# Kernel optimization log

Measured on AMD Instinct MI355X. Metric: run time of the kernel, lower is better.

Reference implementation:

```python
import jax, jax.numpy as jnp
import numpy as np
from jax import lax

EPS = 1e-5

def _layernorm(x, g, b):
    m = jnp.mean(x, axis=-1, keepdims=True)
    v = jnp.mean((x - m) ** 2, axis=-1, keepdims=True)
    return (x - m) * lax.rsqrt(v + EPS) * g + b

def _dwconv(x, H, W, w, b):
    # x: [B, N, C], w: [C, 1, 3, 3] (OIHW, depthwise), b: [C]
    B, N, C = x.shape
    xi = x.transpose(0, 2, 1).reshape(B, C, H, W)
    y = lax.conv_general_dilated(
        xi, w, window_strides=(1, 1), padding='SAME',
        feature_group_count=C,
        dimension_numbers=('NCHW', 'OIHW', 'NCHW'))
    y = y + b[None, :, None, None]
    return y.reshape(B, C, H * W).transpose(0, 2, 1)

def _channel_attn(x, groups, qkv_w, qkv_b, proj_w, proj_b):
    B, N, C = x.shape
    hd = C // groups
    qkv = x @ qkv_w.T + qkv_b                       # [B, N, 3C]
    qkv = qkv.reshape(B, N, 3, groups, hd)
    q, k, v = qkv[:, :, 0], qkv[:, :, 1], qkv[:, :, 2]   # [B, N, g, hd]
    q = q * (float(N) ** -0.5)
    attn = jnp.einsum('bngc,bngd->bgcd', q, k)      # [B, g, hd, hd]
    attn = jax.nn.softmax(attn, axis=-1)
    out = jnp.einsum('bgcd,bngd->bngc', attn, v)    # [B, N, g, hd]
    out = out.reshape(B, N, C)
    return out @ proj_w.T + proj_b

def _block(x, H, W, dw1_w, dw1_b, ln1_g, ln1_b, qkv_w, qkv_b, proj_w, proj_b,
           dw2_w, dw2_b, ln2_g, ln2_b, fc1_w, fc1_b, fc2_w, fc2_b, groups=8):
    # conv1 (no norm) + residual
    x = x + _dwconv(x, H, W, dw1_w, dw1_b)
    # prenorm channel attention + residual
    x = x + _channel_attn(_layernorm(x, ln1_g, ln1_b), groups, qkv_w, qkv_b, proj_w, proj_b)
    # conv2 (no norm) + residual
    x = x + _dwconv(x, H, W, dw2_w, dw2_b)
    # prenorm MLP + residual
    h = _layernorm(x, ln2_g, ln2_b)
    h = jax.nn.gelu(h @ fc1_w.T + fc1_b, approximate=False)
    x = x + (h @ fc2_w.T + fc2_b)
    return x

def setup_inputs() -> dict:
    key = jax.random.key(0)
    B, H, W, C, groups, ratio = 32, 32, 32, 768, 8, 4
    N, Ch = H * W, C * ratio
    ks = jax.random.split(key, 16)
    s = lambda fan: 1.0 / np.sqrt(fan)
    return {
        'x': jax.random.normal(ks[0], (B, N, C), jnp.float32),
        'H': H, 'W': W,
        'dw1_w': jax.random.normal(ks[1], (C, 1, 3, 3), jnp.float32) * s(9),
        'dw1_b': jnp.zeros((C,), jnp.float32),
        'ln1_g': jnp.ones((C,), jnp.float32),
        'ln1_b': jnp.zeros((C,), jnp.float32),
        'qkv_w': jax.random.normal(ks[2], (3 * C, C), jnp.float32) * s(C),
        'qkv_b': jnp.zeros((3 * C,), jnp.float32),
        'proj_w': jax.random.normal(ks[3], (C, C), jnp.float32) * s(C),
        'proj_b': jnp.zeros((C,), jnp.float32),
        'dw2_w': jax.random.normal(ks[4], (C, 1, 3, 3), jnp.float32) * s(9),
        'dw2_b': jnp.zeros((C,), jnp.float32),
        'ln2_g': jnp.ones((C,), jnp.float32),
        'ln2_b': jnp.zeros((C,), jnp.float32),
        'fc1_w': jax.random.normal(ks[5], (Ch, C), jnp.float32) * s(C),
        'fc1_b': jnp.zeros((Ch,), jnp.float32),
        'fc2_w': jax.random.normal(ks[6], (C, Ch), jnp.float32) * s(Ch),
        'fc2_b': jnp.zeros((C,), jnp.float32),
    }

def reference(x, H, W, dw1_w, dw1_b, ln1_g, ln1_b, qkv_w, qkv_b, proj_w, proj_b,
              dw2_w, dw2_b, ln2_g, ln2_b, fc1_w, fc1_b, fc2_w, fc2_b):
    return _block(x, H, W, dw1_w, dw1_b, ln1_g, ln1_b, qkv_w, qkv_b, proj_w, proj_b,
                  dw2_w, dw2_b, ln2_g, ln2_b, fc1_w, fc1_b, fc2_w, fc2_b)
```

## Files before the change

### kernel.cpp

```cpp
#include <hip/hip_runtime.h>

typedef unsigned short ushort_t;
typedef __bf16 v8bf __attribute__((ext_vector_type(8)));
typedef float v4f __attribute__((ext_vector_type(4)));

#define B_ 32
#define N_ 1024
#define C_ 768
#define G_ 8
#define HD_ 96
#define CH_ 3072
#define M_ 32768

static __device__ __forceinline__ float b2f(ushort_t u) {
    union { float f; unsigned int i; } z; z.i = ((unsigned int)u) << 16; return z.f;
}
static __device__ __forceinline__ ushort_t f2b(float f) {
    unsigned int u = __float_as_uint(f);
    u += 0x7fff + ((u >> 16) & 1);
    return (ushort_t)(u >> 16);
}
static __device__ __forceinline__ unsigned int pk2(float a, float b) {
    return (unsigned int)f2b(a) | ((unsigned int)f2b(b) << 16);
}

#define GLOAD_LDS16(g, l) __builtin_amdgcn_global_load_lds( \
    (const __attribute__((address_space(1))) unsigned int*)(g), \
    (__attribute__((address_space(3))) unsigned int*)(l), 16, 0, 0)

__global__ __launch_bounds__(256) void cvt_bf16(
    const float* __restrict__ in, ushort_t* __restrict__ out)
{
    int i = (blockIdx.x * 256 + threadIdx.x) * 4;
    float4 v = *(const float4*)(in + i);
    uint2 p; p.x = pk2(v.x, v.y); p.y = pk2(v.z, v.w);
    *(uint2*)(out + i) = p;
}

__global__ __launch_bounds__(256) void transpose_w(
    const float* __restrict__ w, float* __restrict__ wt)
{
    int i = blockIdx.x * 256 + threadIdx.x;
    int c = i / 9, k = i % 9;
    wt[k * C_ + c] = w[i];
}

__global__ __launch_bounds__(256) void dwconv_add(
    const float* __restrict__ xin, const float* __restrict__ wt,
    const float* __restrict__ bias, float* __restrict__ out)
{
    int t = threadIdx.x;
    int bid = blockIdx.x;
    int cblk = bid % 6;
    int bh = bid / 6;
    int b = bh >> 5, h = bh & 31;
    int tw = t >> 5;
    int c0 = cblk * 128 + (t & 31) * 4;
    int w0 = tw * 4;

    float4 tap[3][6];
#pragma unroll
    for (int dh = 0; dh < 3; dh++) {
        int hh = h + dh - 1;
        bool hok = (hh >= 0) && (hh < 32);
#pragma unroll
        for (int dw = 0; dw < 6; dw++) {
            int ww = w0 + dw - 1;
            bool ok = hok && (ww >= 0) && (ww < 32);
            if (ok)
                tap[dh][dw] = *(const float4*)(
                    xin + (size_t)((b << 10) | (hh << 5) | ww) * C_ + c0);
            else
                tap[dh][dw] = make_float4(0.f, 0.f, 0.f, 0.f);
        }
    }
    float4 wv[9];
#pragma unroll
    for (int k = 0; k < 9; k++)
        wv[k] = *(const float4*)(wt + k * C_ + c0);
    float4 bv = *(const float4*)(bias + c0);

#pragma unroll
    for (int i = 0; i < 4; i++) {
        float4 acc = bv;
#pragma unroll
        for (int dh = 0; dh < 3; dh++)
#pragma unroll
            for (int dw = 0; dw < 3; dw++) {
                float4 xv = tap[dh][i + dw];
                float4 wk = wv[dh * 3 + dw];
                acc.x += wk.x * xv.x; acc.y += wk.y * xv.y;
                acc.z += wk.z * xv.z; acc.w += wk.w * xv.w;
            }
        float4 xr = tap[1][i + 1];
        acc.x += xr.x; acc.y += xr.y; acc.z += xr.z; acc.w += xr.w;
        *(float4*)(out + (size_t)((b << 10) | (h << 5) | (w0 + i)) * C_ + c0) = acc;
    }
}

__global__ __launch_bounds__(256) void layernorm_bf(
    const float* __restrict__ xin, const float* __restrict__ g,
    const float* __restrict__ bb, ushort_t* __restrict__ out)
{
    int row = blockIdx.x;
    int t = threadIdx.x;
    const float* xr = xin + (size_t)row * C_;
    float x0 = xr[t], x1 = xr[t + 256], x2 = xr[t + 512];
    float s1 = x0 + x1 + x2;
    float s2 = x0 * x0 + x1 * x1 + x2 * x2;
#pragma unroll
    for (int o = 32; o > 0; o >>= 1) {
        s1 += __shfl_xor(s1, o);
        s2 += __shfl_xor(s2, o);
    }
    __shared__ float red[8];
    if ((t & 63) == 0) { red[(t >> 6) * 2] = s1; red[(t >> 6) * 2 + 1] = s2; }
    __syncthreads();
    s1 = red[0] + red[2] + red[4] + red[6];
    s2 = red[1] + red[3] + red[5] + red[7];
    float m = s1 * (1.0f / 768.0f);
    float var = s2 * (1.0f / 768.0f) - m * m;
    float inv = rsqrtf(var + 1e-5f);
    ushort_t* orow = out + (size_t)row * C_;
    orow[t]       = f2b((x0 - m) * inv * g[t]       + bb[t]);
    orow[t + 256] = f2b((x1 - m) * inv * g[t + 256] + bb[t + 256]);
    orow[t + 512] = f2b((x2 - m) * inv * g[t + 512] + bb[t + 512]);
}

template <int EPI>
__global__ __launch_bounds__(256) void gemm_bt(
    const ushort_t* __restrict__ A, const ushort_t* __restrict__ W,
    const float* __restrict__ bias, const float* __restrict__ resid,
    void* __restrict__ outv, int M, int Nf, int K)
{
    __shared__ __align__(16) ushort_t ring[3][2][128 * 32];
    int t = threadIdx.x;
    int bm = blockIdx.x;
    int bn = blockIdx.y;
    int wave = t >> 6, lane = t & 63;
    int wm = (wave >> 1) * 64;
    int wn = (wave & 1) * 64;
    int row16 = lane & 15;
    int quad = lane >> 4;
    int qswz = (quad * 8) ^ (((row16 >> 1) & 3) * 8);

    int r0 = wave * 16 + (lane >> 2);
    int r1 = (wave + 4) * 16 + (lane >> 2);
    int c8s = ((lane & 3) ^ ((lane >> 3) & 3)) * 8;
    const ushort_t* Ag0 = A + (size_t)(bm * 128 + r0) * K + c8s;
    const ushort_t* Ag1 = A + (size_t)(bm * 128 + r1) * K + c8s;
    const ushort_t* Wg0 = W + (size_t)(bn * 128 + r0) * K + c8s;
    const ushort_t* Wg1 = W + (size_t)(bn * 128 + r1) * K + c8s;

    v4f acc[4][4];
#pragma unroll
    for (int i = 0; i < 4; i++)
#pragma unroll
        for (int j = 0; j < 4; j++) acc[i][j] = (v4f){0.f, 0.f, 0.f, 0.f};

    const int NT = K >> 5;

    auto STAGE = [&](int kt) {
        int s = kt % 3;
        ushort_t* a = &ring[s][0][0];
        ushort_t* b = &ring[s][1][0];
        int off = kt * 32;
        GLOAD_LDS16(Ag0 + off, a + wave * 512);
        GLOAD_LDS16(Ag1 + off, a + (wave + 4) * 512);
        GLOAD_LDS16(Wg0 + off, b + wave * 512);
        GLOAD_LDS16(Wg1 + off, b + (wave + 4) * 512);
    };

    STAGE(0);
    STAGE(1);
    asm volatile("s_waitcnt vmcnt(4)" ::: "memory");
    __builtin_amdgcn_s_barrier();

    for (int kt = 0; kt < NT; ++kt) {
        if (kt + 2 < NT) STAGE(kt + 2);

        const ushort_t* sA = &ring[kt % 3][0][0];
        const ushort_t* sB = &ring[kt % 3][1][0];
        v8bf af[4], bfr[4];
#pragma unroll
        for (int i = 0; i < 4; i++)
            af[i] = *(const v8bf*)(sA + (wm + i * 16 + row16) * 32 + qswz);
#pragma unroll
        for (int j = 0; j < 4; j++)
            bfr[j] = *(const v8bf*)(sB + (wn + j * 16 + row16) * 32 + qswz);
#pragma unroll
        for (int i = 0; i < 4; i++)
#pragma unroll
            for (int j = 0; j < 4; j++)
                acc[i][j] = __builtin_amdgcn_mfma_f32_16x16x32_bf16(af[i], bfr[j], acc[i][j], 0, 0, 0);

        if (kt + 1 < NT) {
            if (kt + 2 < NT)
                asm volatile("s_waitcnt vmcnt(4)" ::: "memory");
            else
                asm volatile("s_waitcnt vmcnt(0)" ::: "memory");
            __builtin_amdgcn_s_barrier();
        }
    }

#pragma unroll
    for (int i = 0; i < 4; i++) {
#pragma unroll
        for (int j = 0; j < 4; j++) {
            int col = bn * 128 + wn + j * 16 + row16;
            float bv = bias[col];
#pragma unroll
            for (int r = 0; r < 4; r++) {
                int row = bm * 128 + wm + i * 16 + quad * 4 + r;
                float v = acc[i][j][r] + bv;
                if (EPI == 1) v = 0.5f * v * (1.0f + erff(v * 0.70710678118f));
                if (EPI == 2) {
                    v += resid[(size_t)row * Nf + col];
                    ((float*)outv)[(size_t)row * Nf + col] = v;
                } else {
                    ((ushort_t*)outv)[(size_t)row * Nf + col] = f2b(v);
                }
            }
        }
    }
}

__global__ __launch_bounds__(256) void chan_attn(
    const ushort_t* __restrict__ qkv, ushort_t* __restrict__ P)
{
    __shared__ __align__(16) char smem[96 * 97 * 4];
    ushort_t* sQt = (ushort_t*)smem;
    ushort_t* sKt = (ushort_t*)(smem + 96 * 72 * 2);
    float* sS = (float*)smem;
    int bg = blockIdx.x;
    int b = bg >> 3, g = bg & 7;
    int t = threadIdx.x;
    int wave = t >> 6, lane = t & 63;
    int wc = (wave >> 1) * 48, wd = (wave & 1) * 48;
    int row16 = lane & 15, quad = lane >> 4;

    v4f acc[3][3];
#pragma unroll
    for (int i = 0; i < 3; i++)
#pragma unroll
        for (int j = 0; j < 3; j++) acc[i][j] = (v4f){0.f, 0.f, 0.f, 0.f};

    for (int n0 = 0; n0 < N_; n0 += 64) {
        __syncthreads();
#pragma unroll
        for (int i = 0; i < 3; i++) {
            int li = t * 3 + i;
            int r = li / 12, sg = li % 12;
            size_t qoff = ((size_t)(b * N_ + n0 + r) * 3) * C_ + g * HD_ + sg * 8;
            union { uint4 v; ushort_t s[8]; } uq, uk;
            uq.v = *(const uint4*)(qkv + qoff);
            uk.v = *(const uint4*)(qkv + qoff + C_);
#pragma unroll
            for (int k = 0; k < 8; k++) {
                sQt[(sg * 8 + k) * 72 + r] = uq.s[k];
                sKt[(sg * 8 + k) * 72 + r] = uk.s[k];
            }
        }
        __syncthreads();
#pragma unroll
        for (int kk = 0; kk < 64; kk += 32) {
            v8bf af[3], bfr[3];
#pragma unroll
            for (int i = 0; i < 3; i++)
                af[i] = *(const v8bf*)(sQt + (wc + i * 16 + row16) * 72 + kk + quad * 8);
#pragma unroll
            for (int j = 0; j < 3; j++)
                bfr[j] = *(const v8bf*)(sKt + (wd + j * 16 + row16) * 72 + kk + quad * 8);
#pragma unroll
            for (int i = 0; i < 3; i++)
#pragma unroll
                for (int j = 0; j < 3; j++)
                    acc[i][j] = __builtin_amdgcn_mfma_f32_16x16x32_bf16(af[i], bfr[j], acc[i][j], 0, 0, 0);
        }
    }
    __syncthreads();
#pragma unroll
    for (int i = 0; i < 3; i++)
#pragma unroll
        for (int j = 0; j < 3; j++)
#pragma unroll
            for (int r = 0; r < 4; r++) {
                int c = wc + i * 16 + quad * 4 + r;
                int d = wd + j * 16 + row16;
                sS[c * 97 + d] = acc[i][j][r] * 0.03125f;
            }
    __syncthreads();
    if (t < 96) {
        float mx = -1e30f;
        for (int d = 0; d < 96; d++) mx = fmaxf(mx, sS[t * 97 + d]);
        float sum = 0.f;
        for (int d = 0; d < 96; d++) sum += __expf(sS[t * 97 + d] - mx);
        float rs = 1.0f / sum;
        ushort_t* prow = P + (size_t)bg * 9216 + t * 96;
        for (int d = 0; d < 96; d++) prow[d] = f2b(__expf(sS[t * 97 + d] - mx) * rs);
    }
}

__global__ __launch_bounds__(256) void attn_av(
    const ushort_t* __restrict__ qkv, const ushort_t* __restrict__ P,
    ushort_t* __restrict__ out)
{
    __shared__ __align__(16) ushort_t sV[256 * 104];
    __shared__ __align__(16) ushort_t sP[96 * 104];
    int blk = blockIdx.x;
    int nch = blk & 3, g = (blk >> 2) & 7, b = blk >> 5;
    int t = threadIdx.x;
    int n0 = nch * 256;
#pragma unroll
    for (int i = 0; i < 12; i++) {
        int li = t + i * 256;
        int r = li / 12, sg = li % 12;
        size_t voff = ((size_t)(b * N_ + n0 + r) * 3 + 2) * C_ + g * HD_ + sg * 8;
        *(uint4*)(sV + r * 104 + sg * 8) = *(const uint4*)(qkv + voff);
    }
#pragma unroll
    for (int i = 0; i < 5; i++) {
        int li = t + i * 256;
        if (li < 1152) {
            int r = li / 12, sg = li % 12;
            *(uint4*)(sP + r * 104 + sg * 8) =
                *(const uint4*)(P + (size_t)(b * 8 + g) * 9216 + li * 8);
        }
    }
    __syncthreads();
    int wave = t >> 6, lane = t & 63;
    int wm = wave * 64;
    int row16 = lane & 15, quad = lane >> 4;
    v4f acc[4][6];
#pragma unroll
    for (int i = 0; i < 4; i++)
#pragma unroll
        for (int j = 0; j < 6; j++) acc[i][j] = (v4f){0.f, 0.f, 0.f, 0.f};
#pragma unroll
    for (int kk = 0; kk < 96; kk += 32) {
        v8bf af[4], bfr[6];
#pragma unroll
        for (int i = 0; i < 4; i++)
            af[i] = *(const v8bf*)(sV + (wm + i * 16 + row16) * 104 + kk + quad * 8);
#pragma unroll
        for (int j = 0; j < 6; j++)
            bfr[j] = *(const v8bf*)(sP + (j * 16 + row16) * 104 + kk + quad * 8);
#pragma unroll
        for (int i = 0; i < 4; i++)
#pragma unroll
            for (int j = 0; j < 6; j++)
                acc[i][j] = __builtin_amdgcn_mfma_f32_16x16x32_bf16(af[i], bfr[j], acc[i][j], 0, 0, 0);
    }
#pragma unroll
    for (int i = 0; i < 4; i++)
#pragma unroll
        for (int j = 0; j < 6; j++)
#pragma unroll
            for (int r = 0; r < 4; r++) {
                int n = n0 + wm + i * 16 + quad * 4 + r;
                int c = j * 16 + row16;
                out[(size_t)(b * N_ + n) * C_ + g * HD_ + c] = f2b(acc[i][j][r]);
            }
}

extern "C" void kernel_launch(void* const* d_in, const int* in_sizes, int n_in,
                              void* d_out, int out_size, void* d_ws, size_t ws_size,
                              hipStream_t stream)
{
    const float* x      = (const float*)d_in[0];
    const float* dw1_w  = (const float*)d_in[3];
    const float* dw1_b  = (const float*)d_in[4];
    const float* ln1_g  = (const float*)d_in[5];
    const float* ln1_b  = (const float*)d_in[6];
    const float* qkv_w  = (const float*)d_in[7];
    const float* qkv_b  = (const float*)d_in[8];
    const float* proj_w = (const float*)d_in[9];
    const float* proj_b = (const float*)d_in[10];
    const float* dw2_w  = (const float*)d_in[11];
    const float* dw2_b  = (const float*)d_in[12];
    const float* ln2_g  = (const float*)d_in[13];
    const float* ln2_b  = (const float*)d_in[14];
    const float* fc1_w  = (const float*)d_in[15];
    const float* fc1_b  = (const float*)d_in[16];
    const float* fc2_w  = (const float*)d_in[17];
    const float* fc2_b  = (const float*)d_in[18];
    float* outp = (float*)d_out;

    char* ws = (char*)d_ws;
    ushort_t* qkvW = (ushort_t*)ws;
    ushort_t* projW = qkvW + 2304 * 768;
    ushort_t* fc1W = projW + 768 * 768;
    ushort_t* fc2W = fc1W + 3072 * 768;
    const size_t WB = (size_t)(2304*768 + 768*768 + 3072*768 + 768*3072) * 2;
    float* wt1 = (float*)(ws + WB);
    float* wt2 = wt1 + 9 * C_;
    const size_t WTB = 2 * 9 * C_ * sizeof(float);

    size_t CB = 32;
    while (CB > 1 && WB + WTB + CB * 12730368ull > ws_size) CB >>= 1;
    const size_t R = CB * 1024;
    char* act = ws + WB + WTB;
    ushort_t* L  = (ushort_t*)act;
    ushort_t* Ab = (ushort_t*)(act + R * C_ * 2);
    float*    X2 = (float*)(act + 2 * R * C_ * 2);
    ushort_t* P  = (ushort_t*)(act + 2 * R * C_ * 2 + R * C_ * 4);
    ushort_t* D  = (ushort_t*)(act + 2 * R * C_ * 2 + R * C_ * 4 + CB * 147456);

    cvt_bf16<<<2304 * 768 / 1024, 256, 0, stream>>>(qkv_w, qkvW);
    cvt_bf16<<<768 * 768 / 1024, 256, 0, stream>>>(proj_w, projW);
    cvt_bf16<<<3072 * 768 / 1024, 256, 0, stream>>>(fc1_w, fc1W);
    cvt_bf16<<<768 * 3072 / 1024, 256, 0, stream>>>(fc2_w, fc2W);
    transpose_w<<<27, 256, 0, stream>>>(dw1_w, wt1);
    transpose_w<<<27, 256, 0, stream>>>(dw2_w, wt2);

    dwconv_add<<<32 * 32 * 6, 256, 0, stream>>>(x, wt1, dw1_b, outp);

    const int nchunk = (int)(32 / CB);
    for (int c = 0; c < nchunk; c++) {
        float* xc = outp + (size_t)c * R * C_;
        layernorm_bf<<<(int)R, 256, 0, stream>>>(xc, ln1_g, ln1_b, L);
        gemm_bt<0><<<dim3((int)R / 128, 2304 / 128), 256, 0, stream>>>(
            L, qkvW, qkv_b, nullptr, D, (int)R, 2304, C_);
        chan_attn<<<(int)CB * 8, 256, 0, stream>>>(D, P);
        attn_av<<<(int)CB * 32, 256, 0, stream>>>(D, P, Ab);
        gemm_bt<2><<<dim3((int)R / 128, C_ / 128), 256, 0, stream>>>(
            Ab, projW, proj_b, xc, X2, (int)R, C_, C_);
        dwconv_add<<<(int)(R / 1024) * 32 * 6, 256, 0, stream>>>(X2, wt2, dw2_b, xc);
        layernorm_bf<<<(int)R, 256, 0, stream>>>(xc, ln2_g, ln2_b, L);
        gemm_bt<1><<<dim3((int)R / 128, CH_ / 128), 256, 0, stream>>>(
            L, fc1W, fc1_b, nullptr, D, (int)R, CH_, C_);
        gemm_bt<2><<<dim3((int)R / 128, C_ / 128), 256, 0, stream>>>(
            D, fc2W, fc2_b, xc, xc, (int)R, C_, CH_);
    }
}
```

Baseline: 1.181 ms.

## Fuse channel-attention softmax with AV product and batch weight-prep launches

Merges the QK^T/softmax kernel and the attention-times-V kernel into one kernel per (batch, group), keeping the softmax probabilities in shared memory instead of writing them to global memory and reading them back. The Q/K and V loads are register-prefetched one tile ahead to overlap global loads with MFMA work. The four weight-conversion launches and two transpose launches are also folded into single launches. In exchange, the AV phase now runs on only 256 blocks (previously 1024) that loop over N sequentially, which reduces parallelism for that stage.

```diff
diff --git a/kernel.cpp b/kernel.cpp
--- a/kernel.cpp
+++ b/kernel.cpp
@@ -28,19 +28,31 @@
     (const __attribute__((address_space(1))) unsigned int*)(g), \
     (__attribute__((address_space(3))) unsigned int*)(l), 16, 0, 0)
 
-__global__ __launch_bounds__(256) void cvt_bf16(
-    const float* __restrict__ in, ushort_t* __restrict__ out)
-{
-    int i = (blockIdx.x * 256 + threadIdx.x) * 4;
-    float4 v = *(const float4*)(in + i);
+__global__ __launch_bounds__(256) void cvt_all(
+    const float* __restrict__ a, const float* __restrict__ b,
+    const float* __restrict__ c, const float* __restrict__ d,
+    ushort_t* __restrict__ o)
+{
+    int blk = blockIdx.x;
+    const float* src; ushort_t* dst; int off;
+    if (blk < 1728)      { src = a; dst = o;                          off = blk; }
+    else if (blk < 2304) { src = b; dst = o + 2304 * 768;             off = blk - 1728; }
+    else if (blk < 4608) { src = c; dst = o + 2304 * 768 + 768 * 768; off = blk - 2304; }
+    else                 { src = d; dst = o + 2304 * 768 + 768 * 768 + 3072 * 768; off = blk - 4608; }
+    int i = (off * 256 + threadIdx.x) * 4;
+    float4 v = *(const float4*)(src + i);
     uint2 p; p.x = pk2(v.x, v.y); p.y = pk2(v.z, v.w);
-    *(uint2*)(out + i) = p;
-}
-
-__global__ __launch_bounds__(256) void transpose_w(
-    const float* __restrict__ w, float* __restrict__ wt)
-{
-    int i = blockIdx.x * 256 + threadIdx.x;
+    *(uint2*)(dst + i) = p;
+}
+
+__global__ __launch_bounds__(256) void transpose_w2(
+    const float* __restrict__ w1, const float* __restrict__ w2,
+    float* __restrict__ wt1, float* __restrict__ wt2)
+{
+    int blk = blockIdx.x;
+    const float* w = (blk < 27) ? w1 : w2;
+    float* wt = (blk < 27) ? wt1 : wt2;
+    int i = (blk % 27) * 256 + threadIdx.x;
     int c = i / 9, k = i % 9;
     wt[k * C_ + c] = w[i];
 }
@@ -225,13 +237,16 @@
     }
 }
 
-__global__ __launch_bounds__(256) void chan_attn(
-    const ushort_t* __restrict__ qkv, ushort_t* __restrict__ P)
-{
-    __shared__ __align__(16) char smem[96 * 97 * 4];
+__global__ __launch_bounds__(256) void attn_fused(
+    const ushort_t* __restrict__ qkv, ushort_t* __restrict__ out)
+{
+    __shared__ __align__(16) char smem[57216];
     ushort_t* sQt = (ushort_t*)smem;
-    ushort_t* sKt = (ushort_t*)(smem + 96 * 72 * 2);
-    float* sS = (float*)smem;
+    ushort_t* sKt = (ushort_t*)(smem + 13824);
+    float*    sS  = (float*)smem;
+    ushort_t* sP  = (ushort_t*)(smem + 37248);
+    ushort_t* sV  = (ushort_t*)smem;
+
     int bg = blockIdx.x;
     int b = bg >> 3, g = bg & 7;
     int t = threadIdx.x;
@@ -239,45 +254,69 @@
     int wc = (wave >> 1) * 48, wd = (wave & 1) * 48;
     int row16 = lane & 15, quad = lane >> 4;
 
+    int li0 = t * 3;
+    int r_[3], sg_[3];
+#pragma unroll
+    for (int i = 0; i < 3; i++) { r_[i] = (li0 + i) / 12; sg_[i] = (li0 + i) % 12; }
+
     v4f acc[3][3];
 #pragma unroll
     for (int i = 0; i < 3; i++)
 #pragma unroll
         for (int j = 0; j < 3; j++) acc[i][j] = (v4f){0.f, 0.f, 0.f, 0.f};
 
+    uint4 uq[3], uk[3];
+#pragma unroll
+    for (int i = 0; i < 3; i++) {
+        const ushort_t* p = qkv + ((size_t)(b * N_ + r_[i]) * 3) * C_ + g * HD_ + sg_[i] * 8;
+        uq[i] = *(const uint4*)p;
+        uk[i] = *(const uint4*)(p + C_);
+    }
+
     for (int n0 = 0; n0 < N_; n0 += 64) {
+        uint4 nq[3] = {}, nk[3] = {};
+        bool more = (n0 + 64 < N_);
+        if (more) {
+#pragma unroll
+            for (int i = 0; i < 3; i++) {
+                const ushort_t* p = qkv + ((size_t)(b * N_ + n0 + 64 + r_[i]) * 3) * C_ + g * HD_ + sg_[i] * 8;
+                nq[i] = *(const uint4*)p;
+                nk[i] = *(const uint4*)(p + C_);
+            }
+        }
         __syncthreads();
 #pragma unroll
         for (int i = 0; i < 3; i++) {
-            int li = t * 3 + i;
-            int r = li / 12, sg = li % 12;
-            size_t qoff = ((size_t)(b * N_ + n0 + r) * 3) * C_ + g * HD_ + sg * 8;
-            union { uint4 v; ushort_t s[8]; } uq, uk;
-            uq.v = *(const uint4*)(qkv + qoff);
-            uk.v = *(const uint4*)(qkv + qoff + C_);
-#pragma unroll
-            for (int k = 0; k < 8; k++) {
-                sQt[(sg * 8 + k) * 72 + r] = uq.s[k];
-                sKt[(sg * 8 + k) * 72 + r] = uk.s[k];
+            union { uint4 v; ushort_t s[8]; } a, bu;
+            a.v = uq[i]; bu.v = uk[i];
+#pragma unroll
+            for (int k2 = 0; k2 < 8; k2++) {
+                sQt[(sg_[i] * 8 + k2) * 72 + r_[i]] = a.s[k2];
+                sKt[(sg_[i] * 8 + k2) * 72 + r_[i]] = bu.s[k2];
             }
         }
         __syncthreads();
 #pragma unroll
         for (int kk = 0; kk < 64; kk += 32) {
-            v8bf af[3], bfr[3];
+            v8bf af[3], bf2[3];
 #pragma unroll
             for (int i = 0; i < 3; i++)
                 af[i] = *(const v8bf*)(sQt + (wc + i * 16 + row16) * 72 + kk + quad * 8);
 #pragma unroll
             for (int j = 0; j < 3; j++)
-                bfr[j] = *(const v8bf*)(sKt + (wd + j * 16 + row16) * 72 + kk + quad * 8);
+                bf2[j] = *(const v8bf*)(sKt + (wd + j * 16 + row16) * 72 + kk + quad * 8);
 #pragma unroll
             for (int i = 0; i < 3; i++)
 #pragma unroll
                 for (int j = 0; j < 3; j++)
-                    acc[i][j] = __builtin_amdgcn_mfma_f32_16x16x32_bf16(af[i], bfr[j], acc[i][j], 0, 0, 0);
-        }
-    }
+                    acc[i][j] = __builtin_amdgcn_mfma_f32_16x16x32_bf16(af[i], bf2[j], acc[i][j], 0, 0, 0);
+        }
+        if (more) {
+#pragma unroll
+            for (int i = 0; i < 3; i++) { uq[i] = nq[i]; uk[i] = nk[i]; }
+        }
+    }
+
     __syncthreads();
 #pragma unroll
     for (int i = 0; i < 3; i++)
@@ -292,75 +331,70 @@
     __syncthreads();
     if (t < 96) {
         float mx = -1e30f;
+#pragma unroll 8
         for (int d = 0; d < 96; d++) mx = fmaxf(mx, sS[t * 97 + d]);
         float sum = 0.f;
+#pragma unroll 8
         for (int d = 0; d < 96; d++) sum += __expf(sS[t * 97 + d] - mx);
         float rs = 1.0f / sum;
-        ushort_t* prow = P + (size_t)bg * 9216 + t * 96;
-        for (int d = 0; d < 96; d++) prow[d] = f2b(__expf(sS[t * 97 + d] - mx) * rs);
-    }
-}
-
-__global__ __launch_bounds__(256) void attn_av(
-    const ushort_t* __restrict__ qkv, const ushort_t* __restrict__ P,
-    ushort_t* __restrict__ out)
-{
-    __shared__ __align__(16) ushort_t sV[256 * 104];
-    __shared__ __align__(16) ushort_t sP[96 * 104];
-    int blk = blockIdx.x;
-    int nch = blk & 3, g = (blk >> 2) & 7, b = blk >> 5;
-    int t = threadIdx.x;
-    int n0 = nch * 256;
-#pragma unroll
-    for (int i = 0; i < 12; i++) {
-        int li = t + i * 256;
-        int r = li / 12, sg = li % 12;
-        size_t voff = ((size_t)(b * N_ + n0 + r) * 3 + 2) * C_ + g * HD_ + sg * 8;
-        *(uint4*)(sV + r * 104 + sg * 8) = *(const uint4*)(qkv + voff);
-    }
-#pragma unroll
-    for (int i = 0; i < 5; i++) {
-        int li = t + i * 256;
-        if (li < 1152) {
-            int r = li / 12, sg = li % 12;
-            *(uint4*)(sP + r * 104 + sg * 8) =
-                *(const uint4*)(P + (size_t)(b * 8 + g) * 9216 + li * 8);
-        }
+#pragma unroll 8
+        for (int d = 0; d < 96; d++)
+            sP[t * 104 + d] = f2b(__expf(sS[t * 97 + d] - mx) * rs);
     }
     __syncthreads();
-    int wave = t >> 6, lane = t & 63;
-    int wm = wave * 64;
-    int row16 = lane & 15, quad = lane >> 4;
-    v4f acc[4][6];
-#pragma unroll
-    for (int i = 0; i < 4; i++)
-#pragma unroll
-        for (int j = 0; j < 6; j++) acc[i][j] = (v4f){0.f, 0.f, 0.f, 0.f};
-#pragma unroll
-    for (int kk = 0; kk < 96; kk += 32) {
-        v8bf af[4], bfr[6];
-#pragma unroll
-        for (int i = 0; i < 4; i++)
-            af[i] = *(const v8bf*)(sV + (wm + i * 16 + row16) * 104 + kk + quad * 8);
+
+    v8bf pf[3][6];
+#pragma unroll
+    for (int kk = 0; kk < 3; kk++)
 #pragma unroll
         for (int j = 0; j < 6; j++)
-            bfr[j] = *(const v8bf*)(sP + (j * 16 + row16) * 104 + kk + quad * 8);
-#pragma unroll
-        for (int i = 0; i < 4; i++)
+            pf[kk][j] = *(const v8bf*)(sP + (j * 16 + row16) * 104 + kk * 32 + quad * 8);
+
+    int li = t;
+    int vr_[3], vsg_[3];
+#pragma unroll
+    for (int i = 0; i < 3; i++) { vr_[i] = (li + i * 256) / 12; vsg_[i] = (li + i * 256) % 12; }
+
+    uint4 uv[3];
+#pragma unroll
+    for (int i = 0; i < 3; i++)
+        uv[i] = *(const uint4*)(qkv + ((size_t)(b * N_ + vr_[i]) * 3 + 2) * C_ + g * HD_ + vsg_[i] * 8);
+
+    for (int n0 = 0; n0 < N_; n0 += 64) {
+        uint4 nv[3] = {};
+        bool more = (n0 + 64 < N_);
+        if (more) {
+#pragma unroll
+            for (int i = 0; i < 3; i++)
+                nv[i] = *(const uint4*)(qkv + ((size_t)(b * N_ + n0 + 64 + vr_[i]) * 3 + 2) * C_ + g * HD_ + vsg_[i] * 8);
+        }
+        __syncthreads();
+#pragma unroll
+        for (int i = 0; i < 3; i++)
+            *(uint4*)(sV + vr_[i] * 104 + vsg_[i] * 8) = uv[i];
+        __syncthreads();
+        v4f a2[6];
+#pragma unroll
+        for (int j = 0; j < 6; j++) a2[j] = (v4f){0.f, 0.f, 0.f, 0.f};
+#pragma unroll
+        for (int kk = 0; kk < 3; kk++) {
+            v8bf av = *(const v8bf*)(sV + (wave * 16 + row16) * 104 + kk * 32 + quad * 8);
 #pragma unroll
             for (int j = 0; j < 6; j++)
-                acc[i][j] = __builtin_amdgcn_mfma_f32_16x16x32_bf16(af[i], bfr[j], acc[i][j], 0, 0, 0);
-    }
-#pragma unroll
-    for (int i = 0; i < 4; i++)
+                a2[j] = __builtin_amdgcn_mfma_f32_16x16x32_bf16(av, pf[kk][j], a2[j], 0, 0, 0);
+        }
 #pragma unroll
         for (int j = 0; j < 6; j++)
 #pragma unroll
-            for (int r = 0; r < 4; r++) {
-                int n = n0 + wm + i * 16 + quad * 4 + r;
-                int c = j * 16 + row16;
-                out[(size_t)(b * N_ + n) * C_ + g * HD_ + c] = f2b(acc[i][j][r]);
-            }
+            for (int rr = 0; rr < 4; rr++) {
+                int n = n0 + wave * 16 + quad * 4 + rr;
+                out[(size_t)(b * N_ + n) * C_ + g * HD_ + j * 16 + row16] = f2b(a2[j][rr]);
+            }
+        if (more) {
+#pragma unroll
+            for (int i = 0; i < 3; i++) uv[i] = nv[i];
+        }
+    }
 }
 
 extern "C" void kernel_launch(void* const* d_in, const int* in_sizes, int n_in,
@@ -403,15 +437,10 @@
     ushort_t* L  = (ushort_t*)act;
     ushort_t* Ab = (ushort_t*)(act + R * C_ * 2);
     float*    X2 = (float*)(act + 2 * R * C_ * 2);
-    ushort_t* P  = (ushort_t*)(act + 2 * R * C_ * 2 + R * C_ * 4);
     ushort_t* D  = (ushort_t*)(act + 2 * R * C_ * 2 + R * C_ * 4 + CB * 147456);
 
-    cvt_bf16<<<2304 * 768 / 1024, 256, 0, stream>>>(qkv_w, qkvW);
-    cvt_bf16<<<768 * 768 / 1024, 256, 0, stream>>>(proj_w, projW);
-    cvt_bf16<<<3072 * 768 / 1024, 256, 0, stream>>>(fc1_w, fc1W);
-    cvt_bf16<<<768 * 3072 / 1024, 256, 0, stream>>>(fc2_w, fc2W);
-    transpose_w<<<27, 256, 0, stream>>>(dw1_w, wt1);
-    transpose_w<<<27, 256, 0, stream>>>(dw2_w, wt2);
+    cvt_all<<<6912, 256, 0, stream>>>(qkv_w, proj_w, fc1_w, fc2_w, qkvW);
+    transpose_w2<<<54, 256, 0, stream>>>(dw1_w, dw2_w, wt1, wt2);
 
     dwconv_add<<<32 * 32 * 6, 256, 0, stream>>>(x, wt1, dw1_b, outp);
 
@@ -421,8 +450,7 @@
         layernorm_bf<<<(int)R, 256, 0, stream>>>(xc, ln1_g, ln1_b, L);
         gemm_bt<0><<<dim3((int)R / 128, 2304 / 128), 256, 0, stream>>>(
             L, qkvW, qkv_b, nullptr, D, (int)R, 2304, C_);
-        chan_attn<<<(int)CB * 8, 256, 0, stream>>>(D, P);
-        attn_av<<<(int)CB * 32, 256, 0, stream>>>(D, P, Ab);
+        attn_fused<<<(int)CB * 8, 256, 0, stream>>>(D, Ab);
         gemm_bt<2><<<dim3((int)R / 128, C_ / 128), 256, 0, stream>>>(
             Ab, projW, proj_b, xc, X2, (int)R, C_, C_);
         dwconv_add<<<(int)(R / 1024) * 32 * 6, 256, 0, stream>>>(X2, wt2, dw2_b, xc);
```

Result: slower. 1.220 ms (+3.3%).
